# Kernel optimization log

Measured on AMD Instinct MI355X. Metric: run time of the kernel, lower is better.

Reference implementation:

```python
import jax, jax.numpy as jnp
import numpy as np

B, T, H = 64, 32, 768          # batch, num query tokens, hidden
E, NB, DFF = 8, 2, 3072        # num_experts, num_beams, expert ffn dim


def setup_inputs() -> dict:
    key = jax.random.key(0)
    ks = jax.random.split(key, 6)
    x = jax.random.normal(ks[0], (B, T, H), dtype=jnp.float32)
    gate_w = jax.random.normal(ks[1], (E, H), dtype=jnp.float32) * 0.02
    w1 = jax.random.normal(ks[2], (E, DFF, H), dtype=jnp.float32) * 0.02
    b1 = jnp.zeros((E, DFF), dtype=jnp.float32)
    w2 = jax.random.normal(ks[3], (E, H, DFF), dtype=jnp.float32) * 0.02
    b2 = jnp.zeros((E, H), dtype=jnp.float32)
    return {"x": x, "gate_w": gate_w, "w1": w1, "b1": b1, "w2": w2, "b2": b2}


def reference(x, gate_w, w1, b1, w2, b2):
    # ---- forward_gate: attention_mask is all ones -> plain mean over tokens ----
    x_avg = jnp.mean(x, axis=1)                         # [B, H]
    logits_gate = x_avg @ gate_w.T                      # [B, E]
    current_scores = jax.nn.softmax(logits_gate, axis=-1)

    # ---- importance auxiliary loss (torch.std is unbiased, ddof=1) ----
    importance = jnp.sum(current_scores, axis=0)        # [E]
    importance_loss = (jnp.std(importance, ddof=1) / jnp.mean(importance)) ** 2

    # ---- beam_search, first layer: exp(log(scores)) == scores; topk num_beams ----
    topk_vals, topk_idx = jax.lax.top_k(current_scores, NB)   # [B, NB]
    beam_scores = topk_vals.reshape(B * NB)
    expert_route = topk_idx.reshape(B * NB, 1).astype(jnp.int32)
    beam_idx = jnp.arange(B * NB, dtype=jnp.int32)

    # ---- replicate x / scores per beam: unsqueeze+expand+view == repeat ----
    x_rep = jnp.repeat(x, NB, axis=0)                   # [B*NB, T, H]
    scores_rep = jnp.repeat(current_scores, NB, axis=0) # [B*NB, E]
    input_x = x_rep[beam_idx]                           # identity gather (faithful)

    # ---- forward_expert_ffn: run ALL experts, then one-hot * prob combine ----
    h = jnp.einsum('bth,efh->betf', input_x, w1) + b1[None, :, None, :]
    h = jax.nn.gelu(h, approximate=False)               # torch nn.GELU default (exact)
    cand = jnp.einsum('betf,ehf->beth', h, w2) + b2[None, :, None, :]  # [B*NB, E, T, H]

    sel = expert_route[:, -1]                           # [B*NB]
    onehot = jax.nn.one_hot(sel, E, dtype=cand.dtype)   # [B*NB, E]
    weights = scores_rep * onehot                       # weight_type == 'ffn_prob'
    output = jnp.einsum('beth,be->bth', cand, weights)  # [B*NB, T, H]

    return output, beam_scores, expert_route, beam_idx, importance_loss
```

## Files before the change

kernel.cpp:

```cpp
#include <hip/hip_runtime.h>
#include <hip/hip_bf16.h>
#include <math.h>

#define Bsz 64
#define T 32
#define H 768
#define E 8
#define NB 2
#define DFF 3072
#define NBEAM (Bsz * NB)
#define NT4MAX 40

#define OUT_BS 3145728
#define OUT_ER 3145856
#define OUT_BI 3145984
#define OUT_IL 3146112

#define WS_LOGITS 0
#define WS_BEAMW  512
#define WS_SORT   768
#define WS_T4E    896
#define WS_T4B    936
#define WS_T4C    976
#define WS_XBF    1024
#define WS_HBF    (1024 + 786432)

typedef __attribute__((ext_vector_type(8))) short short8;
typedef __attribute__((ext_vector_type(4))) float f32x4;

__device__ __forceinline__ short8 cvt8(const float4 u, const float4 v) {
    union { short8 s; unsigned w[4]; } r;
    __hip_bfloat162 t;
    t = __float22bfloat162_rn(make_float2(u.x, u.y)); r.w[0] = *(unsigned*)&t;
    t = __float22bfloat162_rn(make_float2(u.z, u.w)); r.w[1] = *(unsigned*)&t;
    t = __float22bfloat162_rn(make_float2(v.x, v.y)); r.w[2] = *(unsigned*)&t;
    t = __float22bfloat162_rn(make_float2(v.z, v.w)); r.w[3] = *(unsigned*)&t;
    return r.s;
}

__device__ __forceinline__ void async16(void* lds, const void* g) {
    __builtin_amdgcn_global_load_lds(
        (const __attribute__((address_space(1))) void*)g,
        (__attribute__((address_space(3))) void*)lds, 16, 0, 0);
}

__global__ __launch_bounds__(256) void gate_logits_kernel(
    const float* __restrict__ x, const float* __restrict__ gate_w,
    float* __restrict__ logits, ushort* __restrict__ xb)
{
    __shared__ float avg[H];
    const int b = blockIdx.x, tid = threadIdx.x;
    for (int c = tid; c < H; c += 256) {
        const float* xp = x  + (size_t)b * T * H + c;
        ushort*      xo = xb + (size_t)b * T * H + c;
        float s = 0.f;
        #pragma unroll
        for (int t = 0; t < T; ++t) {
            const float v = xp[t * H];
            s += v;
            __hip_bfloat16 hb = __float2bfloat16(v);
            xo[t * H] = *(ushort*)&hb;
        }
        avg[c] = s * (1.0f / T);
    }
    __syncthreads();
    const int e = tid >> 5, l = tid & 31;
    float p = 0.f;
    for (int c = l; c < H; c += 32) p += avg[c] * gate_w[e * H + c];
    #pragma unroll
    for (int off = 16; off; off >>= 1) p += __shfl_down(p, off, 32);
    if (l == 0) logits[b * E + e] = p;
}

__global__ __launch_bounds__(64) void gating_kernel(
    const float* __restrict__ logits, float* __restrict__ beam_w,
    int* __restrict__ sortb, int* __restrict__ t4e, int* __restrict__ t4b,
    int* __restrict__ t4c, float* __restrict__ dout)
{
    __shared__ float sc[Bsz][E];
    __shared__ int sexp[NBEAM];
    const int r = threadIdx.x;
    float v[E];
    float mx = -1e30f;
    #pragma unroll
    for (int e = 0; e < E; ++e) { v[e] = logits[r * E + e]; mx = fmaxf(mx, v[e]); }
    float s = 0.f;
    #pragma unroll
    for (int e = 0; e < E; ++e) { v[e] = expf(v[e] - mx); s += v[e]; }
    const float inv = 1.0f / s;
    #pragma unroll
    for (int e = 0; e < E; ++e) { v[e] *= inv; sc[r][e] = v[e]; }
    float v0 = -1.f, v1 = -1.f; int i0 = 0, i1 = 0;
    #pragma unroll
    for (int e = 0; e < E; ++e) {
        if (v[e] > v0)      { v1 = v0; i1 = i0; v0 = v[e]; i0 = e; }
        else if (v[e] > v1) { v1 = v[e]; i1 = e; }
    }
    const int b0 = 2 * r, b1 = 2 * r + 1;
    dout[OUT_BS + b0] = v0;          dout[OUT_BS + b1] = v1;
    dout[OUT_ER + b0] = (float)i0;   dout[OUT_ER + b1] = (float)i1;
    dout[OUT_BI + b0] = (float)b0;   dout[OUT_BI + b1] = (float)b1;
    beam_w[b0] = v0;  beam_w[b1] = v1;
    sexp[b0] = i0;    sexp[b1] = i1;
    __syncthreads();
    if (r == 0) {
        float imp[E]; float tot = 0.f;
        #pragma unroll
        for (int e = 0; e < E; ++e) {
            float a = 0.f;
            for (int rr = 0; rr < Bsz; ++rr) a += sc[rr][e];
            imp[e] = a; tot += a;
        }
        const float mean = tot / E;
        float var = 0.f;
        #pragma unroll
        for (int e = 0; e < E; ++e) { float d = imp[e] - mean; var += d * d; }
        var /= (E - 1);
        dout[OUT_IL] = var / (mean * mean);
        int cntE[E]; int offE[E]; int posE[E];
        #pragma unroll
        for (int e = 0; e < E; ++e) cntE[e] = 0;
        for (int b = 0; b < NBEAM; ++b) cntE[sexp[b]]++;
        int a0 = 0;
        #pragma unroll
        for (int e = 0; e < E; ++e) { offE[e] = a0; posE[e] = a0; a0 += cntE[e]; }
        for (int b = 0; b < NBEAM; ++b) sortb[posE[sexp[b]]++] = b;
        int t = 0;
        for (int e = 0; e < E; ++e) {
            for (int i = 0; i < cntE[e]; i += 4) {
                t4e[t] = e;
                t4b[t] = offE[e] + i;
                t4c[t] = (cntE[e] - i < 4) ? (cntE[e] - i) : 4;
                ++t;
            }
        }
        for (; t < NT4MAX; ++t) t4c[t] = 0;
    }
}

template <int KTOT, int NTILE, bool DO_GELU>
__global__ __launch_bounds__(256) void moe_ffn_mfma(
    const ushort* __restrict__ Abf, int a_div,
    const float* __restrict__ Wf32, int w_rows,
    const float* __restrict__ biasb,
    const int* __restrict__ sortb, const int* __restrict__ t4e,
    const int* __restrict__ t4b, const int* __restrict__ t4c,
    const float* __restrict__ beam_w,
    void* __restrict__ Obase)
{
    constexpr int KT = KTOT / 64;
    constexpr int WF = NTILE / 32;
    __shared__ __align__(16) ushort sA[128 * 64];
    __shared__ __align__(16) ushort sB[NTILE * 64];

    const int tile = blockIdx.y;
    const int cnt  = t4c[tile];
    if (cnt == 0) return;
    const int e    = t4e[tile];
    const int base = t4b[tile];
    const int tid  = threadIdx.x;
    const int wv   = tid >> 6;
    const int lane = tid & 63;
    const int quad = lane >> 4;
    const int l16  = lane & 15;
    const int mh   = (wv & 1) * 64;
    const int nh   = (wv >> 1) * (NTILE / 2);
    const int n0   = blockIdx.x * NTILE;

    int bm[4];
    #pragma unroll
    for (int s = 0; s < 4; ++s) bm[s] = sortb[base + (s < cnt ? s : cnt - 1)];

    const ushort* aseg[4];
    #pragma unroll
    for (int jj = 0; jj < 4; ++jj) {
        const int j = wv * 4 + jj;
        const int s = j * 64 + lane;
        const int r = s >> 3;
        const int c = (s & 7) ^ (r & 7);
        aseg[jj] = Abf + (size_t)(bm[r >> 5] / a_div) * T * KTOT
                 + (size_t)(r & 31) * KTOT + c * 8;
    }
    const float* wseg[WF];
    int wslot[WF];
    #pragma unroll
    for (int jj = 0; jj < WF; ++jj) {
        const int s = jj * 256 + tid;
        const int r = s >> 3;
        const int c = (s & 7) ^ (r & 7);
        wseg[jj] = Wf32 + (size_t)e * w_rows * KTOT + (size_t)(n0 + r) * KTOT + c * 8;
        wslot[jj] = s * 8;
    }

    int arow[4], ar7[4], brow[WF], br7[WF];
    #pragma unroll
    for (int mt = 0; mt < 4; ++mt) {
        const int r = mh + mt * 16 + l16;
        arow[mt] = r * 64; ar7[mt] = r & 7;
    }
    #pragma unroll
    for (int nt = 0; nt < WF; ++nt) {
        const int r = nh + nt * 16 + l16;
        brow[nt] = r * 64; br7[nt] = r & 7;
    }

    float4 wr[WF][2];
    #pragma unroll
    for (int jj = 0; jj < WF; ++jj) {
        wr[jj][0] = *(const float4*)(wseg[jj]);
        wr[jj][1] = *(const float4*)(wseg[jj] + 4);
    }
    #pragma unroll
    for (int jj = 0; jj < 4; ++jj)
        async16((char*)sA + (wv * 4 + jj) * 1024, aseg[jj]);

    f32x4 acc[4][WF];
    #pragma unroll
    for (int mt = 0; mt < 4; ++mt)
        #pragma unroll
        for (int nt = 0; nt < WF; ++nt) acc[mt][nt] = {0.f, 0.f, 0.f, 0.f};

    for (int kt = 0; kt < KT; ++kt) {
        #pragma unroll
        for (int jj = 0; jj < WF; ++jj)
            *(short8*)(sB + wslot[jj]) = cvt8(wr[jj][0], wr[jj][1]);
        __syncthreads();
        if (kt + 1 < KT) {
            const int kn = (kt + 1) * 64;
            #pragma unroll
            for (int jj = 0; jj < WF; ++jj) {
                wr[jj][0] = *(const float4*)(wseg[jj] + kn);
                wr[jj][1] = *(const float4*)(wseg[jj] + kn + 4);
            }
        }
        #pragma unroll
        for (int ks = 0; ks < 2; ++ks) {
            short8 af[4], wf[WF];
            #pragma unroll
            for (int mt = 0; mt < 4; ++mt)
                af[mt] = *(const short8*)(sA + arow[mt] + (((ks * 4 + quad) ^ ar7[mt]) * 8));
            #pragma unroll
            for (int nt = 0; nt < WF; ++nt)
                wf[nt] = *(const short8*)(sB + brow[nt] + (((ks * 4 + quad) ^ br7[nt]) * 8));
            #pragma unroll
            for (int mt = 0; mt < 4; ++mt)
                #pragma unroll
                for (int nt = 0; nt < WF; ++nt)
                    acc[mt][nt] = __builtin_amdgcn_mfma_f32_16x16x32_bf16(
                        af[mt], wf[nt], acc[mt][nt], 0, 0, 0);
        }
        if (kt + 1 < KT) {
            __syncthreads();
            const int kn = (kt + 1) * 64;
            #pragma unroll
            for (int jj = 0; jj < 4; ++jj)
                async16((char*)sA + (wv * 4 + jj) * 1024, aseg[jj] + kn);
        }
    }

    #pragma unroll
    for (int nt = 0; nt < WF; ++nt) {
        const int n = n0 + nh + nt * 16 + l16;
        const float bias = biasb[(size_t)e * w_rows + n];
        #pragma unroll
        for (int mt = 0; mt < 4; ++mt) {
            const int rowb = mh + mt * 16 + quad * 4;
            const int s = rowb >> 5;
            if (s >= cnt) continue;
            const int b = bm[s];
            const float scale = DO_GELU ? 1.0f : beam_w[b];
            #pragma unroll
            for (int r = 0; r < 4; ++r) {
                const int t = (rowb + r) & 31;
                float vv = acc[mt][nt][r] + bias;
                const size_t idx = (size_t)b * T * w_rows + (size_t)t * w_rows + n;
                if (DO_GELU) {
                    vv = 0.5f * vv * (1.0f + erff(vv * 0.70710678118654752f));
                    ((__hip_bfloat16*)Obase)[idx] = __float2bfloat16(vv);
                } else {
                    ((float*)Obase)[idx] = vv * scale;
                }
            }
        }
    }
}

extern "C" void kernel_launch(void* const* d_in, const int* in_sizes, int n_in,
                              void* d_out, int out_size, void* d_ws, size_t ws_size,
                              hipStream_t stream)
{
    const float* x      = (const float*)d_in[0];
    const float* gate_w = (const float*)d_in[1];
    const float* w1     = (const float*)d_in[2];
    const float* b1     = (const float*)d_in[3];
    const float* w2     = (const float*)d_in[4];
    const float* b2     = (const float*)d_in[5];
    float* out = (float*)d_out;
    float* ws  = (float*)d_ws;

    float*  logits = ws + WS_LOGITS;
    float*  beam_w = ws + WS_BEAMW;
    int*    sortb  = (int*)(ws + WS_SORT);
    int*    t4e    = (int*)(ws + WS_T4E);
    int*    t4b    = (int*)(ws + WS_T4B);
    int*    t4c    = (int*)(ws + WS_T4C);
    ushort* x_bf   = (ushort*)(ws + WS_XBF);
    ushort* h_bf   = (ushort*)(ws + WS_HBF);

    gate_logits_kernel<<<Bsz, 256, 0, stream>>>(x, gate_w, logits, x_bf);
    gating_kernel<<<1, 64, 0, stream>>>(logits, beam_w, sortb, t4e, t4b, t4c, out);
    moe_ffn_mfma<H, 128, true><<<dim3(DFF / 128, NT4MAX), 256, 0, stream>>>(
        x_bf, NB, w1, DFF, b1, sortb, t4e, t4b, t4c, beam_w, (void*)h_bf);
    moe_ffn_mfma<DFF, 64, false><<<dim3(H / 64, NT4MAX), 256, 0, stream>>>(
        h_bf, 1, w2, H, b2, sortb, t4e, t4b, t4c, beam_w, out);
}
```

Baseline: 316.6 us.

## Split gate prologue, parallelize gating with ballots, double-buffer MoE GEMM LDS

The gate kernel is split in two: a vectorized kernel converts x to bf16, and a separate kernel computes the gate logits as 3 partial sums per batch, so the work spreads over more blocks. The gating kernel now computes importance with wave shuffles and builds the expert sort and tile lists with ballot and popcount, replacing the serial single-thread loops. The MFMA FFN kernel double-buffers its A and B LDS tiles, so the next A tile's async load is issued before the current compute and one barrier per k-step is removed. It also adds a min-2-blocks launch bound. In exchange, LDS use doubles, register pressure may rise, and x is now read twice by two separate kernels.

```diff
diff --git a/kernel.cpp b/kernel.cpp
--- a/kernel.cpp
+++ b/kernel.cpp
@@ -17,13 +17,13 @@
 #define OUT_IL 3146112
 
 #define WS_LOGITS 0
-#define WS_BEAMW  512
-#define WS_SORT   768
-#define WS_T4E    896
-#define WS_T4B    936
-#define WS_T4C    976
-#define WS_XBF    1024
-#define WS_HBF    (1024 + 786432)
+#define WS_BEAMW  1536
+#define WS_SORT   1664
+#define WS_T4E    1792
+#define WS_T4B    1832
+#define WS_T4C    1872
+#define WS_XBF    2048
+#define WS_HBF    (2048 + 786432)
 
 typedef __attribute__((ext_vector_type(8))) short short8;
 typedef __attribute__((ext_vector_type(4))) float f32x4;
@@ -44,52 +44,67 @@
         (__attribute__((address_space(3))) void*)lds, 16, 0, 0);
 }
 
-__global__ __launch_bounds__(256) void gate_logits_kernel(
+__global__ __launch_bounds__(256) void conv_x_kernel(
+    const float* __restrict__ x, ushort* __restrict__ xb, int n4)
+{
+    const int i = blockIdx.x * 256 + threadIdx.x;
+    if (i >= n4) return;
+    const float4 v = ((const float4*)x)[i];
+    __hip_bfloat162 t0 = __float22bfloat162_rn(make_float2(v.x, v.y));
+    __hip_bfloat162 t1 = __float22bfloat162_rn(make_float2(v.z, v.w));
+    ushort4 o;
+    o.x = (*(unsigned*)&t0) & 0xffff; o.y = (*(unsigned*)&t0) >> 16;
+    o.z = (*(unsigned*)&t1) & 0xffff; o.w = (*(unsigned*)&t1) >> 16;
+    ((ushort4*)xb)[i] = o;
+}
+
+__global__ __launch_bounds__(256) void gate_partial_kernel(
     const float* __restrict__ x, const float* __restrict__ gate_w,
-    float* __restrict__ logits, ushort* __restrict__ xb)
-{
-    __shared__ float avg[H];
-    const int b = blockIdx.x, tid = threadIdx.x;
-    for (int c = tid; c < H; c += 256) {
-        const float* xp = x  + (size_t)b * T * H + c;
-        ushort*      xo = xb + (size_t)b * T * H + c;
-        float s = 0.f;
-        #pragma unroll
-        for (int t = 0; t < T; ++t) {
-            const float v = xp[t * H];
-            s += v;
-            __hip_bfloat16 hb = __float2bfloat16(v);
-            xo[t * H] = *(ushort*)&hb;
-        }
-        avg[c] = s * (1.0f / T);
+    float* __restrict__ logits_part)
+{
+    __shared__ float part[4][E];
+    const int chunk = blockIdx.x, b = blockIdx.y;
+    const int tid = threadIdx.x, wv = tid >> 6, lane = tid & 63;
+    const int c = chunk * 256 + tid;
+    const float* xp = x + (size_t)b * T * H + c;
+    float s = 0.f;
+    #pragma unroll
+    for (int t = 0; t < T; ++t) s += xp[t * H];
+    const float avg = s * (1.0f / T);
+    #pragma unroll
+    for (int e = 0; e < E; ++e) {
+        float p = avg * gate_w[e * H + c];
+        #pragma unroll
+        for (int off = 32; off; off >>= 1) p += __shfl_down(p, off, 64);
+        if (lane == 0) part[wv][e] = p;
     }
     __syncthreads();
-    const int e = tid >> 5, l = tid & 31;
-    float p = 0.f;
-    for (int c = l; c < H; c += 32) p += avg[c] * gate_w[e * H + c];
-    #pragma unroll
-    for (int off = 16; off; off >>= 1) p += __shfl_down(p, off, 32);
-    if (l == 0) logits[b * E + e] = p;
+    if (tid < E) {
+        float t = part[0][tid] + part[1][tid] + part[2][tid] + part[3][tid];
+        logits_part[chunk * 512 + b * E + tid] = t;
+    }
 }
 
 __global__ __launch_bounds__(64) void gating_kernel(
-    const float* __restrict__ logits, float* __restrict__ beam_w,
+    const float* __restrict__ logits_part, float* __restrict__ beam_w,
     int* __restrict__ sortb, int* __restrict__ t4e, int* __restrict__ t4b,
     int* __restrict__ t4c, float* __restrict__ dout)
 {
-    __shared__ float sc[Bsz][E];
-    __shared__ int sexp[NBEAM];
     const int r = threadIdx.x;
     float v[E];
     float mx = -1e30f;
     #pragma unroll
-    for (int e = 0; e < E; ++e) { v[e] = logits[r * E + e]; mx = fmaxf(mx, v[e]); }
+    for (int e = 0; e < E; ++e) {
+        v[e] = logits_part[r * E + e] + logits_part[512 + r * E + e]
+             + logits_part[1024 + r * E + e];
+        mx = fmaxf(mx, v[e]);
+    }
     float s = 0.f;
     #pragma unroll
     for (int e = 0; e < E; ++e) { v[e] = expf(v[e] - mx); s += v[e]; }
     const float inv = 1.0f / s;
     #pragma unroll
-    for (int e = 0; e < E; ++e) { v[e] *= inv; sc[r][e] = v[e]; }
+    for (int e = 0; e < E; ++e) v[e] *= inv;
     float v0 = -1.f, v1 = -1.f; int i0 = 0, i1 = 0;
     #pragma unroll
     for (int e = 0; e < E; ++e) {
@@ -101,45 +116,61 @@
     dout[OUT_ER + b0] = (float)i0;   dout[OUT_ER + b1] = (float)i1;
     dout[OUT_BI + b0] = (float)b0;   dout[OUT_BI + b1] = (float)b1;
     beam_w[b0] = v0;  beam_w[b1] = v1;
-    sexp[b0] = i0;    sexp[b1] = i1;
-    __syncthreads();
+    float imp[E];
+    #pragma unroll
+    for (int e = 0; e < E; ++e) {
+        float t = v[e];
+        #pragma unroll
+        for (int off = 1; off < 64; off <<= 1) t += __shfl_xor(t, off, 64);
+        imp[e] = t;
+    }
     if (r == 0) {
-        float imp[E]; float tot = 0.f;
-        #pragma unroll
-        for (int e = 0; e < E; ++e) {
-            float a = 0.f;
-            for (int rr = 0; rr < Bsz; ++rr) a += sc[rr][e];
-            imp[e] = a; tot += a;
-        }
+        float tot = 0.f;
+        #pragma unroll
+        for (int e = 0; e < E; ++e) tot += imp[e];
         const float mean = tot / E;
         float var = 0.f;
         #pragma unroll
         for (int e = 0; e < E; ++e) { float d = imp[e] - mean; var += d * d; }
         var /= (E - 1);
         dout[OUT_IL] = var / (mean * mean);
-        int cntE[E]; int offE[E]; int posE[E];
-        #pragma unroll
-        for (int e = 0; e < E; ++e) cntE[e] = 0;
-        for (int b = 0; b < NBEAM; ++b) cntE[sexp[b]]++;
-        int a0 = 0;
-        #pragma unroll
-        for (int e = 0; e < E; ++e) { offE[e] = a0; posE[e] = a0; a0 += cntE[e]; }
-        for (int b = 0; b < NBEAM; ++b) sortb[posE[sexp[b]]++] = b;
-        int t = 0;
-        for (int e = 0; e < E; ++e) {
-            for (int i = 0; i < cntE[e]; i += 4) {
-                t4e[t] = e;
-                t4b[t] = offE[e] + i;
-                t4c[t] = (cntE[e] - i < 4) ? (cntE[e] - i) : 4;
-                ++t;
-            }
+    }
+    unsigned long long m0[E], m1[E];
+    #pragma unroll
+    for (int e = 0; e < E; ++e) {
+        m0[e] = __ballot(i0 == e);
+        m1[e] = __ballot(i1 == e);
+    }
+    int cnt[E], off[E];
+    int a0 = 0;
+    #pragma unroll
+    for (int e = 0; e < E; ++e) {
+        cnt[e] = __popcll(m0[e]) + __popcll(m1[e]);
+        off[e] = a0; a0 += cnt[e];
+    }
+    const unsigned long long below = (r == 0) ? 0ull : ((1ull << r) - 1ull);
+    const unsigned long long incl  = below | (1ull << r);
+    const int pos0 = __popcll(m0[i0] & below) + __popcll(m1[i0] & below);
+    const int pos1 = __popcll(m0[i1] & incl)  + __popcll(m1[i1] & below);
+    sortb[off[i0] + pos0] = b0;
+    sortb[off[i1] + pos1] = b1;
+    int tb[E]; int tc = 0;
+    #pragma unroll
+    for (int e = 0; e < E; ++e) { tb[e] = tc; tc += (cnt[e] + 3) >> 2; }
+    if (r < E) {
+        const int e = r;
+        int j = tb[e];
+        for (int i = 0; i < cnt[e]; i += 4, ++j) {
+            t4e[j] = e;
+            t4b[j] = off[e] + i;
+            t4c[j] = (cnt[e] - i < 4) ? (cnt[e] - i) : 4;
         }
-        for (; t < NT4MAX; ++t) t4c[t] = 0;
-    }
+    }
+    for (int t = tc + r; t < NT4MAX; t += 64) t4c[t] = 0;
 }
 
 template <int KTOT, int NTILE, bool DO_GELU>
-__global__ __launch_bounds__(256) void moe_ffn_mfma(
+__global__ __launch_bounds__(256, 2) void moe_ffn_mfma(
     const ushort* __restrict__ Abf, int a_div,
     const float* __restrict__ Wf32, int w_rows,
     const float* __restrict__ biasb,
@@ -150,8 +181,8 @@
 {
     constexpr int KT = KTOT / 64;
     constexpr int WF = NTILE / 32;
-    __shared__ __align__(16) ushort sA[128 * 64];
-    __shared__ __align__(16) ushort sB[NTILE * 64];
+    __shared__ __align__(16) ushort sA[2][128 * 64];
+    __shared__ __align__(16) ushort sB[2][NTILE * 64];
 
     const int tile = blockIdx.y;
     const int cnt  = t4c[tile];
@@ -174,8 +205,7 @@
     const ushort* aseg[4];
     #pragma unroll
     for (int jj = 0; jj < 4; ++jj) {
-        const int j = wv * 4 + jj;
-        const int s = j * 64 + lane;
+        const int s = (wv * 4 + jj) * 64 + lane;
         const int r = s >> 3;
         const int c = (s & 7) ^ (r & 7);
         aseg[jj] = Abf + (size_t)(bm[r >> 5] / a_div) * T * KTOT
@@ -212,7 +242,7 @@
     }
     #pragma unroll
     for (int jj = 0; jj < 4; ++jj)
-        async16((char*)sA + (wv * 4 + jj) * 1024, aseg[jj]);
+        async16((char*)sA[0] + (wv * 4 + jj) * 1024, aseg[jj]);
 
     f32x4 acc[4][WF];
     #pragma unroll
@@ -221,12 +251,16 @@
         for (int nt = 0; nt < WF; ++nt) acc[mt][nt] = {0.f, 0.f, 0.f, 0.f};
 
     for (int kt = 0; kt < KT; ++kt) {
+        const int p = kt & 1;
         #pragma unroll
         for (int jj = 0; jj < WF; ++jj)
-            *(short8*)(sB + wslot[jj]) = cvt8(wr[jj][0], wr[jj][1]);
+            *(short8*)(sB[p] + wslot[jj]) = cvt8(wr[jj][0], wr[jj][1]);
         __syncthreads();
         if (kt + 1 < KT) {
             const int kn = (kt + 1) * 64;
+            #pragma unroll
+            for (int jj = 0; jj < 4; ++jj)
+                async16((char*)sA[1 - p] + (wv * 4 + jj) * 1024, aseg[jj] + kn);
             #pragma unroll
             for (int jj = 0; jj < WF; ++jj) {
                 wr[jj][0] = *(const float4*)(wseg[jj] + kn);
@@ -238,23 +272,16 @@
             short8 af[4], wf[WF];
             #pragma unroll
             for (int mt = 0; mt < 4; ++mt)
-                af[mt] = *(const short8*)(sA + arow[mt] + (((ks * 4 + quad) ^ ar7[mt]) * 8));
+                af[mt] = *(const short8*)(sA[p] + arow[mt] + (((ks * 4 + quad) ^ ar7[mt]) * 8));
             #pragma unroll
             for (int nt = 0; nt < WF; ++nt)
-                wf[nt] = *(const short8*)(sB + brow[nt] + (((ks * 4 + quad) ^ br7[nt]) * 8));
+                wf[nt] = *(const short8*)(sB[p] + brow[nt] + (((ks * 4 + quad) ^ br7[nt]) * 8));
             #pragma unroll
             for (int mt = 0; mt < 4; ++mt)
                 #pragma unroll
                 for (int nt = 0; nt < WF; ++nt)
                     acc[mt][nt] = __builtin_amdgcn_mfma_f32_16x16x32_bf16(
                         af[mt], wf[nt], acc[mt][nt], 0, 0, 0);
-        }
-        if (kt + 1 < KT) {
-            __syncthreads();
-            const int kn = (kt + 1) * 64;
-            #pragma unroll
-            for (int jj = 0; jj < 4; ++jj)
-                async16((char*)sA + (wv * 4 + jj) * 1024, aseg[jj] + kn);
         }
     }
 
@@ -307,7 +334,9 @@
     ushort* x_bf   = (ushort*)(ws + WS_XBF);
     ushort* h_bf   = (ushort*)(ws + WS_HBF);
 
-    gate_logits_kernel<<<Bsz, 256, 0, stream>>>(x, gate_w, logits, x_bf);
+    conv_x_kernel<<<(Bsz * T * H / 4 + 255) / 256, 256, 0, stream>>>(
+        x, x_bf, Bsz * T * H / 4);
+    gate_partial_kernel<<<dim3(3, Bsz), 256, 0, stream>>>(x, gate_w, logits);
     gating_kernel<<<1, 64, 0, stream>>>(logits, beam_w, sortb, t4e, t4b, t4c, out);
     moe_ffn_mfma<H, 128, true><<<dim3(DFF / 128, NT4MAX), 256, 0, stream>>>(
         x_bf, NB, w1, DFF, b1, sortb, t4e, t4b, t4c, beam_w, (void*)h_bf);
```

New measurement: 306.7 us. 1.03x faster.
